# Kernel optimization log

Hardware: AMD Instinct MI355X
Metric: run time of the kernel (lower is better)

The kernel has to match this reference:

```python
import jax, jax.numpy as jnp
import numpy as np

B, T, D, H, E = 2, 1024, 1024, 4096, 8


def setup_inputs() -> dict:
    key = jax.random.key(0)
    ks = jax.random.split(key, 7)
    s = 0.02  # weight init scale
    return {
        "x": jax.random.normal(ks[0], (B, T, D), jnp.float32),
        "gate_w": jax.random.normal(ks[1], (D, E), jnp.float32) * s,
        "gate_b": jnp.zeros((E,), jnp.float32),
        "w1": jax.random.normal(ks[2], (E, D, H), jnp.float32) * s,
        "b1": jnp.zeros((E, H), jnp.float32),
        "w2": jax.random.normal(ks[3], (E, H, D), jnp.float32) * s,
        "b2": jnp.zeros((E, D), jnp.float32),
    }


def reference(x, gate_w, gate_b, w1, b1, w2, b2):
    b, t, d = x.shape
    e = gate_w.shape[1]
    xt = x.reshape(b * t, d)                      # [N, D]
    logits = xt @ gate_w + gate_b                 # [N, E]
    probs = jax.nn.softmax(logits, axis=-1)
    top_expert = jnp.argmax(probs, axis=-1)       # [N]
    onehot = jax.nn.one_hot(top_expert, e, dtype=x.dtype)  # [N, E]
    # dense per-expert FFN, then combine via top-1 one-hot (same math as masked dispatch)
    h = jax.nn.gelu(jnp.einsum('nd,edh->enh', xt, w1) + b1[:, None, :], approximate=False)  # [E, N, H]
    y = jnp.einsum('enh,ehd->end', h, w2) + b2[:, None, :]                                  # [E, N, D]
    out = jnp.einsum('end,ne->nd', y, onehot).reshape(b, t, d)
    counts = jnp.sum(onehot, axis=0)              # [E], float
    frac = counts / jnp.maximum(counts.sum(), 1.0)
    aux_loss = jnp.mean((frac - 1.0 / e) ** 2)
    return out, aux_loss
```

## Files before the change

kernel.cpp:

```cpp
#include <hip/hip_runtime.h>
#include <stdint.h>

#define N_TOK 2048
#define DDIM 1024
#define HDIM 4096
#define NEXP 8
#define BM 128
#define MAXT 24
#define PADCAP 3072

#define C_COUNTS 0
#define C_CURSOR 8
#define C_PADOFF 16
#define C_TILECNT 25
#define C_TILE_E 32
#define C_TILE_M0 56
#define C_TILE_ROWS 80
#define C_EXPERT 128
#define C_PERM 2176

#define XG_OFF 32768
#define HG_OFF (XG_OFF + PADCAP*DDIM*2)

typedef float f32x4 __attribute__((ext_vector_type(4)));
typedef short s16x8 __attribute__((ext_vector_type(8)));
typedef unsigned int u32;
typedef unsigned short u16;

__device__ __forceinline__ u16 f2bf(float f){
  u32 u = __float_as_uint(f);
  u += 0x7fffu + ((u >> 16) & 1u);
  return (u16)(u >> 16);
}

__device__ __forceinline__ u32 pkbf(float a, float b){
  u32 r; asm("v_cvt_pk_bf16_f32 %0, %1, %2" : "=v"(r) : "v"(a), "v"(b)); return r;
}

__device__ __forceinline__ void gl_lds16(const void* g, void* l){
  __builtin_amdgcn_global_load_lds((const __attribute__((address_space(1))) u32*)g,
                                   (__attribute__((address_space(3))) u32*)l, 16, 0, 0);
}

__global__ __launch_bounds__(256) void gate_kern(
    const float* __restrict__ x, const float* __restrict__ gw,
    const float* __restrict__ gb, int* __restrict__ ctrl)
{
  const int wv = threadIdx.x >> 6, l = threadIdx.x & 63;
  const int n = blockIdx.x * 4 + wv;
  const float* xr = x + (size_t)n * DDIM;
  float acc[NEXP];
  #pragma unroll
  for (int e = 0; e < NEXP; e++) acc[e] = 0.f;
  #pragma unroll 4
  for (int i = 0; i < DDIM/64; i++){
    int k = i*64 + l;
    float xv = xr[k];
    const float* g = gw + (size_t)k * NEXP;
    #pragma unroll
    for (int e = 0; e < NEXP; e++) acc[e] = fmaf(xv, g[e], acc[e]);
  }
  #pragma unroll
  for (int e = 0; e < NEXP; e++){
    #pragma unroll
    for (int off = 32; off > 0; off >>= 1) acc[e] += __shfl_xor(acc[e], off);
  }
  if (l == 0){
    float best = acc[0] + gb[0]; int bi = 0;
    #pragma unroll
    for (int e = 1; e < NEXP; e++){
      float v = acc[e] + gb[e];
      if (v > best){ best = v; bi = e; }
    }
    ctrl[C_EXPERT + n] = bi;
    atomicAdd(&ctrl[C_COUNTS + bi], 1);
  }
}

__global__ void setup_kern(int* __restrict__ ctrl, float* __restrict__ aux_out)
{
  const int t = threadIdx.x;
  for (int i = t; i < PADCAP; i += 256) ctrl[C_PERM + i] = -1;
  if (t == 0){
    int off = 0, tc = 0;
    float aux = 0.f;
    for (int e = 0; e < NEXP; e++){
      int c = ctrl[C_COUNTS + e];
      ctrl[C_PADOFF + e] = off;
      ctrl[C_CURSOR + e] = off;
      int nt = (c + BM - 1) / BM;
      for (int j = 0; j < nt; j++){
        ctrl[C_TILE_E   + tc] = e;
        ctrl[C_TILE_M0  + tc] = off + j*BM;
        ctrl[C_TILE_ROWS+ tc] = min(BM, c - j*BM);
        tc++;
      }
      off += nt * BM;
      float fr = (float)c * (1.f/(float)N_TOK);
      float d = fr - 1.f/(float)NEXP;
      aux += d*d;
    }
    ctrl[C_TILECNT] = tc;
    *aux_out = aux * (1.f/(float)NEXP);
  }
}

__global__ __launch_bounds__(256) void scatter_kern(int* __restrict__ ctrl)
{
  const int n = blockIdx.x * 256 + threadIdx.x;
  const int e = ctrl[C_EXPERT + n];
  const int pos = atomicAdd(&ctrl[C_CURSOR + e], 1);
  ctrl[C_PERM + pos] = n;
}

__global__ __launch_bounds__(256) void xg_kern(
    const float* __restrict__ x, const int* __restrict__ ctrl,
    u16* __restrict__ Xg)
{
  const int slot = blockIdx.x, t = threadIdx.x;
  const int tok = ctrl[C_PERM + slot];
  ushort4 o;
  if (tok >= 0){
    f32x4 v = *(const f32x4*)(x + (size_t)tok*DDIM + t*4);
    o.x = f2bf(v.x); o.y = f2bf(v.y); o.z = f2bf(v.z); o.w = f2bf(v.w);
  } else { o.x = 0; o.y = 0; o.z = 0; o.w = 0; }
  *(ushort4*)(Xg + (size_t)slot*DDIM + t*4) = o;
}

template<int MODE>
__global__ __launch_bounds__(256, 4) void moe_gemm(
    const u16* __restrict__ Ag, const float* __restrict__ W,
    const float* __restrict__ bias, u16* __restrict__ Hg,
    float* __restrict__ outp, const int* __restrict__ ctrl)
{
  constexpr int K    = (MODE==1) ? DDIM : HDIM;
  constexpr int NN   = (MODE==1) ? HDIM : DDIM;
  constexpr int KS   = (MODE==1) ? 1 : 4;
  constexpr int KLOC = K / KS;
  constexpr int BN   = 64;
  constexpr int BK   = 32;
  constexpr int NF   = BN / 32;
  constexpr int CPR  = BK / 8;
  constexpr int AVM  = (BM*BK)/(256*8);
  constexpr int BCPR = BN / 4;
  constexpr int BVM  = (BK*BN)/(256*4);
  constexpr int NT   = KLOC / BK;

  const int by = blockIdx.y;
  if (by >= ctrl[C_TILECNT]) return;
  const int e    = ctrl[C_TILE_E + by];
  const int m0   = ctrl[C_TILE_M0 + by];
  const int rows = ctrl[C_TILE_ROWS + by];
  const int n0   = blockIdx.x * BN;
  const int kb   = (MODE==1) ? 0 : blockIdx.z * KLOC;

  const int tid = threadIdx.x;
  const int w = tid >> 6, l = tid & 63;
  const int wr = w >> 1, wc = w & 1;
  const int lhi = l >> 4, llo = l & 15;

  __shared__ __align__(16) u16   As[2][BM*BK];
  __shared__ __align__(16) float Bs[2][BK*BN];
  __shared__ int perm_s[BM];

  if constexpr (MODE == 2){
    if (tid < BM) perm_s[tid] = ctrl[C_PERM + m0 + tid];
  }

  f32x4 acc[4][NF];
  #pragma unroll
  for (int mf = 0; mf < 4; mf++)
    #pragma unroll
    for (int nf = 0; nf < NF; nf++) acc[mf][nf] = (f32x4){0.f,0.f,0.f,0.f};

  const u16* Abase = Ag + (size_t)m0 * K;
  int arow[AVM], apos[AVM];
  #pragma unroll
  for (int i = 0; i < AVM; i++){
    int f = i*256 + tid;
    arow[i] = f / CPR;
    apos[i] = (f & (CPR-1)) ^ (arow[i] & (CPR-1));
  }
  const float* Wb = W + (size_t)e * K * NN + n0;
  int brow[BVM], bpos[BVM];
  #pragma unroll
  for (int i = 0; i < BVM; i++){
    int f = i*256 + tid;
    brow[i] = f / BCPR;
    bpos[i] = (f % BCPR) ^ (((brow[i] >> 3) & 1) << 2);
  }

  const int col0 = wc*(BN/2) + llo;
  const int bswz = (lhi & 1) << 2;

#define STAGE_A(buf, k0) { \
    u16* ad = &As[buf][(w*64)*8]; \
    _Pragma("unroll") \
    for (int i = 0; i < AVM; i++) \
      gl_lds16(Abase + (size_t)arow[i]*K + (k0) + apos[i]*8, ad + i*256*8); }

#define STAGE_B(buf, k0) { \
    float* bd = &Bs[buf][(w*64)*4]; \
    _Pragma("unroll") \
    for (int i = 0; i < BVM; i++) \
      gl_lds16(Wb + (size_t)((k0) + brow[i])*NN + bpos[i]*4, bd + i*256*4); }

#define COMPUTE(buf) { \
    s16x8 a[4]; \
    _Pragma("unroll") \
    for (int mf = 0; mf < 4; mf++){ \
      int row = wr*64 + mf*16 + llo; \
      int pos = lhi ^ (row & (CPR-1)); \
      a[mf] = *(const s16x8*)&As[buf][row*BK + pos*8]; } \
    _Pragma("unroll") \
    for (int nf = 0; nf < NF; nf++){ \
      const int col = col0 + nf*16; \
      const float* bp_ = &Bs[buf][(lhi*8)*BN + \
                                  ((((col) >> 2) ^ bswz) << 2) + ((col) & 3)]; \
      union { u32 u[4]; s16x8 v; } bb_; \
      bb_.u[0] = pkbf(bp_[0*BN], bp_[1*BN]); \
      bb_.u[1] = pkbf(bp_[2*BN], bp_[3*BN]); \
      bb_.u[2] = pkbf(bp_[4*BN], bp_[5*BN]); \
      bb_.u[3] = pkbf(bp_[6*BN], bp_[7*BN]); \
      _Pragma("unroll") \
      for (int mf = 0; mf < 4; mf++) \
        acc[mf][nf] = __builtin_amdgcn_mfma_f32_16x16x32_bf16(a[mf], bb_.v, acc[mf][nf], 0, 0, 0); \
    } }

  STAGE_A(0, kb);
  STAGE_B(0, kb);
  __syncthreads();

  int cur = 0;
  #pragma unroll 1
  for (int t = 0; t < NT; t++){
    if (t+1 < NT){
      STAGE_A(cur^1, kb + (t+1)*BK);
      STAGE_B(cur^1, kb + (t+1)*BK);
    }
    COMPUTE(cur);
    __syncthreads();
    cur ^= 1;
  }

  if constexpr (MODE == 1){
    const float* bp = bias + (size_t)e*NN + n0;
    #pragma unroll
    for (int nf = 0; nf < NF; nf++){
      const int cl = wc*(BN/2) + nf*16 + llo;
      const float bb = bp[cl];
      #pragma unroll
      for (int mf = 0; mf < 4; mf++){
        #pragma unroll
        for (int r = 0; r < 4; r++){
          const int rl = wr*64 + mf*16 + lhi*4 + r;
          float vv = acc[mf][nf][r] + bb;
          float gel = 0.5f * vv * (1.0f + erff(vv * 0.70710678118f));
          Hg[(size_t)(m0+rl)*NN + n0 + cl] = f2bf(gel);
        }
      }
    }
  } else {
    const float* bp = bias + (size_t)e*NN + n0;
    const bool addb = (blockIdx.z == 0);
    #pragma unroll
    for (int mf = 0; mf < 4; mf++){
      #pragma unroll
      for (int r = 0; r < 4; r++){
        const int rl = wr*64 + mf*16 + lhi*4 + r;
        if (rl < rows){
          const int tok = perm_s[rl];
          #pragma unroll
          for (int nf = 0; nf < NF; nf++){
            const int cl = wc*(BN/2) + nf*16 + llo;
            float v = acc[mf][nf][r] + (addb ? bp[cl] : 0.f);
            atomicAdd(&outp[(size_t)tok*DDIM + n0 + cl], v);
          }
        }
      }
    }
  }
#undef STAGE_A
#undef STAGE_B
#undef COMPUTE
}

extern "C" void kernel_launch(void* const* d_in, const int* in_sizes, int n_in,
                              void* d_out, int out_size, void* d_ws, size_t ws_size,
                              hipStream_t stream)
{
  (void)in_sizes; (void)n_in; (void)out_size; (void)ws_size;
  const float* x  = (const float*)d_in[0];
  const float* gw = (const float*)d_in[1];
  const float* gb = (const float*)d_in[2];
  const float* w1 = (const float*)d_in[3];
  const float* b1 = (const float*)d_in[4];
  const float* w2 = (const float*)d_in[5];
  const float* b2 = (const float*)d_in[6];
  float* out = (float*)d_out;
  char* ws = (char*)d_ws;
  int* ctrl = (int*)ws;
  u16* Xg = (u16*)(ws + XG_OFF);
  u16* Hg = (u16*)(ws + HG_OFF);

  hipMemsetAsync(ctrl, 0, 64, stream);
  hipMemsetAsync(out, 0, (size_t)N_TOK*DDIM*4, stream);
  gate_kern<<<N_TOK/4, 256, 0, stream>>>(x, gw, gb, ctrl);
  setup_kern<<<1, 256, 0, stream>>>(ctrl, out + (size_t)N_TOK*DDIM);
  scatter_kern<<<N_TOK/256, 256, 0, stream>>>(ctrl);
  xg_kern<<<PADCAP, 256, 0, stream>>>(x, ctrl, Xg);
  moe_gemm<1><<<dim3(HDIM/64, MAXT),    256, 0, stream>>>(Xg, w1, b1, Hg, nullptr, ctrl);
  moe_gemm<2><<<dim3(DDIM/64, MAXT, 4), 256, 0, stream>>>(Hg, w2, b2, nullptr, out, ctrl);
}
```

Measured before the change: 238.4 us.

## Load GEMM operands directly from global into registers, dropping LDS staging

```diff
diff --git a/kernel.cpp b/kernel.cpp
--- a/kernel.cpp
+++ b/kernel.cpp
@@ -35,11 +35,6 @@
 
 __device__ __forceinline__ u32 pkbf(float a, float b){
   u32 r; asm("v_cvt_pk_bf16_f32 %0, %1, %2" : "=v"(r) : "v"(a), "v"(b)); return r;
-}
-
-__device__ __forceinline__ void gl_lds16(const void* g, void* l){
-  __builtin_amdgcn_global_load_lds((const __attribute__((address_space(1))) u32*)g,
-                                   (__attribute__((address_space(3))) u32*)l, 16, 0, 0);
 }
 
 __global__ __launch_bounds__(256) void gate_kern(
@@ -128,7 +123,7 @@
 }
 
 template<int MODE>
-__global__ __launch_bounds__(256, 4) void moe_gemm(
+__global__ __launch_bounds__(256, 3) void moe_gemm(
     const u16* __restrict__ Ag, const float* __restrict__ W,
     const float* __restrict__ bias, u16* __restrict__ Hg,
     float* __restrict__ outp, const int* __restrict__ ctrl)
@@ -140,10 +135,6 @@
   constexpr int BN   = 64;
   constexpr int BK   = 32;
   constexpr int NF   = BN / 32;
-  constexpr int CPR  = BK / 8;
-  constexpr int AVM  = (BM*BK)/(256*8);
-  constexpr int BCPR = BN / 4;
-  constexpr int BVM  = (BK*BN)/(256*4);
   constexpr int NT   = KLOC / BK;
 
   const int by = blockIdx.y;
@@ -159,95 +150,59 @@
   const int wr = w >> 1, wc = w & 1;
   const int lhi = l >> 4, llo = l & 15;
 
-  __shared__ __align__(16) u16   As[2][BM*BK];
-  __shared__ __align__(16) float Bs[2][BK*BN];
-  __shared__ int perm_s[BM];
-
-  if constexpr (MODE == 2){
-    if (tid < BM) perm_s[tid] = ctrl[C_PERM + m0 + tid];
-  }
-
   f32x4 acc[4][NF];
   #pragma unroll
   for (int mf = 0; mf < 4; mf++)
     #pragma unroll
     for (int nf = 0; nf < NF; nf++) acc[mf][nf] = (f32x4){0.f,0.f,0.f,0.f};
 
-  const u16* Abase = Ag + (size_t)m0 * K;
-  int arow[AVM], apos[AVM];
-  #pragma unroll
-  for (int i = 0; i < AVM; i++){
-    int f = i*256 + tid;
-    arow[i] = f / CPR;
-    apos[i] = (f & (CPR-1)) ^ (arow[i] & (CPR-1));
-  }
-  const float* Wb = W + (size_t)e * K * NN + n0;
-  int brow[BVM], bpos[BVM];
-  #pragma unroll
-  for (int i = 0; i < BVM; i++){
-    int f = i*256 + tid;
-    brow[i] = f / BCPR;
-    bpos[i] = (f % BCPR) ^ (((brow[i] >> 3) & 1) << 2);
-  }
-
-  const int col0 = wc*(BN/2) + llo;
-  const int bswz = (lhi & 1) << 2;
-
-#define STAGE_A(buf, k0) { \
-    u16* ad = &As[buf][(w*64)*8]; \
+  const u16* Arow = Ag + (size_t)(m0 + wr*64 + llo) * K + lhi*8;
+  const float* Wc = W + (size_t)e * K * NN + n0 + wc*32 + llo;
+
+  s16x8 af0[4], af1[4];
+  float bw0[NF*8], bw1[NF*8];
+
+#define LOADA(AF, k0) { \
     _Pragma("unroll") \
-    for (int i = 0; i < AVM; i++) \
-      gl_lds16(Abase + (size_t)arow[i]*K + (k0) + apos[i]*8, ad + i*256*8); }
-
-#define STAGE_B(buf, k0) { \
-    float* bd = &Bs[buf][(w*64)*4]; \
-    _Pragma("unroll") \
-    for (int i = 0; i < BVM; i++) \
-      gl_lds16(Wb + (size_t)((k0) + brow[i])*NN + bpos[i]*4, bd + i*256*4); }
-
-#define COMPUTE(buf) { \
-    s16x8 a[4]; \
-    _Pragma("unroll") \
-    for (int mf = 0; mf < 4; mf++){ \
-      int row = wr*64 + mf*16 + llo; \
-      int pos = lhi ^ (row & (CPR-1)); \
-      a[mf] = *(const s16x8*)&As[buf][row*BK + pos*8]; } \
+    for (int mf = 0; mf < 4; mf++) \
+      AF[mf] = *(const s16x8*)(Arow + (size_t)mf*16*K + (k0)); }
+
+#define LOADB(BW, k0) { \
     _Pragma("unroll") \
     for (int nf = 0; nf < NF; nf++){ \
-      const int col = col0 + nf*16; \
-      const float* bp_ = &Bs[buf][(lhi*8)*BN + \
-                                  ((((col) >> 2) ^ bswz) << 2) + ((col) & 3)]; \
+      const float* wp = Wc + (size_t)((k0) + lhi*8) * NN + nf*16; \
+      _Pragma("unroll") \
+      for (int j = 0; j < 8; j++) \
+        BW[nf*8+j] = wp[(size_t)j * NN]; } }
+
+#define COMP(AF, BW) { \
+    _Pragma("unroll") \
+    for (int nf = 0; nf < NF; nf++){ \
       union { u32 u[4]; s16x8 v; } bb_; \
-      bb_.u[0] = pkbf(bp_[0*BN], bp_[1*BN]); \
-      bb_.u[1] = pkbf(bp_[2*BN], bp_[3*BN]); \
-      bb_.u[2] = pkbf(bp_[4*BN], bp_[5*BN]); \
-      bb_.u[3] = pkbf(bp_[6*BN], bp_[7*BN]); \
+      bb_.u[0] = pkbf(BW[nf*8+0], BW[nf*8+1]); \
+      bb_.u[1] = pkbf(BW[nf*8+2], BW[nf*8+3]); \
+      bb_.u[2] = pkbf(BW[nf*8+4], BW[nf*8+5]); \
+      bb_.u[3] = pkbf(BW[nf*8+6], BW[nf*8+7]); \
       _Pragma("unroll") \
       for (int mf = 0; mf < 4; mf++) \
-        acc[mf][nf] = __builtin_amdgcn_mfma_f32_16x16x32_bf16(a[mf], bb_.v, acc[mf][nf], 0, 0, 0); \
-    } }
-
-  STAGE_A(0, kb);
-  STAGE_B(0, kb);
-  __syncthreads();
-
-  int cur = 0;
+        acc[mf][nf] = __builtin_amdgcn_mfma_f32_16x16x32_bf16(AF[mf], bb_.v, acc[mf][nf], 0, 0, 0); } }
+
+  LOADA(af0, kb);
+  LOADB(bw0, kb);
+
   #pragma unroll 1
-  for (int t = 0; t < NT; t++){
-    if (t+1 < NT){
-      STAGE_A(cur^1, kb + (t+1)*BK);
-      STAGE_B(cur^1, kb + (t+1)*BK);
-    }
-    COMPUTE(cur);
-    __syncthreads();
-    cur ^= 1;
+  for (int t = 0; t < NT; t += 2){
+    if (t+1 < NT){ LOADA(af1, kb + (t+1)*BK); LOADB(bw1, kb + (t+1)*BK); }
+    COMP(af0, bw0);
+    if (t+2 < NT){ LOADA(af0, kb + (t+2)*BK); LOADB(bw0, kb + (t+2)*BK); }
+    if (t+1 < NT){ COMP(af1, bw1); }
   }
 
   if constexpr (MODE == 1){
     const float* bp = bias + (size_t)e*NN + n0;
     #pragma unroll
     for (int nf = 0; nf < NF; nf++){
-      const int cl = wc*(BN/2) + nf*16 + llo;
+      const int cl = wc*32 + nf*16 + llo;
       const float bb = bp[cl];
       #pragma unroll
       for (int mf = 0; mf < 4; mf++){
@@ -269,10 +224,10 @@
       for (int r = 0; r < 4; r++){
         const int rl = wr*64 + mf*16 + lhi*4 + r;
         if (rl < rows){
-          const int tok = perm_s[rl];
+          const int tok = ctrl[C_PERM + m0 + rl];
           #pragma unroll
           for (int nf = 0; nf < NF; nf++){
-            const int cl = wc*(BN/2) + nf*16 + llo;
+            const int cl = wc*32 + nf*16 + llo;
             float v = acc[mf][nf][r] + (addb ? bp[cl] : 0.f);
             atomicAdd(&outp[(size_t)tok*DDIM + n0 + cl], v);
           }
@@ -280,9 +235,9 @@
       }
     }
   }
-#undef STAGE_A
-#undef STAGE_B
-#undef COMPUTE
+#undef LOADA
+#undef LOADB
+#undef COMP
 }
 
 extern "C" void kernel_launch(void* const* d_in, const int* in_sizes, int n_in,
```

New measurement: 339.8 us. 1.43x slower.

## Triple-buffer GEMM LDS staging with partial vmcnt waits and MFMA priority

Applied to the files above, without the earlier changes.

```diff
diff --git a/kernel.cpp b/kernel.cpp
--- a/kernel.cpp
+++ b/kernel.cpp
@@ -128,7 +128,7 @@
 }
 
 template<int MODE>
-__global__ __launch_bounds__(256, 4) void moe_gemm(
+__global__ __launch_bounds__(256, 3) void moe_gemm(
     const u16* __restrict__ Ag, const float* __restrict__ W,
     const float* __restrict__ bias, u16* __restrict__ Hg,
     float* __restrict__ outp, const int* __restrict__ ctrl)
@@ -159,8 +159,8 @@
   const int wr = w >> 1, wc = w & 1;
   const int lhi = l >> 4, llo = l & 15;
 
-  __shared__ __align__(16) u16   As[2][BM*BK];
-  __shared__ __align__(16) float Bs[2][BK*BN];
+  __shared__ __align__(16) u16   As[3][BM*BK];
+  __shared__ __align__(16) float Bs[3][BK*BN];
   __shared__ int perm_s[BM];
 
   if constexpr (MODE == 2){
@@ -179,7 +179,7 @@
   for (int i = 0; i < AVM; i++){
     int f = i*256 + tid;
     arow[i] = f / CPR;
-    apos[i] = (f & (CPR-1)) ^ (arow[i] & (CPR-1));
+    apos[i] = (f & (CPR-1)) ^ (arow[i] & (CPR-1)) ^ (((arow[i] >> 2) & 1) << 1);
   }
   const float* Wb = W + (size_t)e * K * NN + n0;
   int brow[BVM], bpos[BVM];
@@ -192,6 +192,12 @@
 
   const int col0 = wc*(BN/2) + llo;
   const int bswz = (lhi & 1) << 2;
+
+#define WAITV(N) asm volatile("s_waitcnt vmcnt(" #N ")" ::: "memory")
+#define PIPE_BAR() do { asm volatile("s_waitcnt lgkmcnt(0)" ::: "memory"); \
+    __builtin_amdgcn_sched_barrier(0); \
+    __builtin_amdgcn_s_barrier(); \
+    __builtin_amdgcn_sched_barrier(0); } while(0)
 
 #define STAGE_A(buf, k0) { \
     u16* ad = &As[buf][(w*64)*8]; \
@@ -210,8 +216,9 @@
     _Pragma("unroll") \
     for (int mf = 0; mf < 4; mf++){ \
       int row = wr*64 + mf*16 + llo; \
-      int pos = lhi ^ (row & (CPR-1)); \
+      int pos = (lhi ^ (row & (CPR-1))) ^ (((row >> 2) & 1) << 1); \
       a[mf] = *(const s16x8*)&As[buf][row*BK + pos*8]; } \
+    __builtin_amdgcn_s_setprio(1); \
     _Pragma("unroll") \
     for (int nf = 0; nf < NF; nf++){ \
       const int col = col0 + nf*16; \
@@ -225,22 +232,28 @@
       _Pragma("unroll") \
       for (int mf = 0; mf < 4; mf++) \
         acc[mf][nf] = __builtin_amdgcn_mfma_f32_16x16x32_bf16(a[mf], bb_.v, acc[mf][nf], 0, 0, 0); \
-    } }
+    } \
+    __builtin_amdgcn_s_setprio(0); }
 
   STAGE_A(0, kb);
   STAGE_B(0, kb);
-  __syncthreads();
-
-  int cur = 0;
+  STAGE_A(1, kb + BK);
+  STAGE_B(1, kb + BK);
+  WAITV(4);
+  PIPE_BAR();
+
+  int cbuf = 0, sbuf = 2;
   #pragma unroll 1
   for (int t = 0; t < NT; t++){
-    if (t+1 < NT){
-      STAGE_A(cur^1, kb + (t+1)*BK);
-      STAGE_B(cur^1, kb + (t+1)*BK);
-    }
-    COMPUTE(cur);
-    __syncthreads();
-    cur ^= 1;
+    if (t+2 < NT){
+      STAGE_A(sbuf, kb + (t+2)*BK);
+      STAGE_B(sbuf, kb + (t+2)*BK);
+    }
+    COMPUTE(cbuf);
+    if (t+2 < NT){ WAITV(4); } else { WAITV(0); }
+    PIPE_BAR();
+    cbuf = (cbuf==2) ? 0 : cbuf+1;
+    sbuf = (sbuf==2) ? 0 : sbuf+1;
   }
 
   if constexpr (MODE == 1){
@@ -280,6 +293,8 @@
       }
     }
   }
+#undef WAITV
+#undef PIPE_BAR
 #undef STAGE_A
 #undef STAGE_B
 #undef COMPUTE
```

Measured after the change: 232.8 us. -2.4%, faster.

## Enlarge MoE GEMM tiles, pack weights to bf16 in LDS, compact token layout

Applied to the files above, without the earlier changes.

```diff
diff --git a/kernel.cpp b/kernel.cpp
--- a/kernel.cpp
+++ b/kernel.cpp
@@ -5,9 +5,9 @@
 #define DDIM 1024
 #define HDIM 4096
 #define NEXP 8
-#define BM 128
-#define MAXT 24
-#define PADCAP 3072
+#define BM 256
+#define MAXT 16
+#define ACAP 2560
 
 #define C_COUNTS 0
 #define C_CURSOR 8
@@ -20,11 +20,12 @@
 #define C_PERM 2176
 
 #define XG_OFF 32768
-#define HG_OFF (XG_OFF + PADCAP*DDIM*2)
+#define HG_OFF (XG_OFF + ACAP*DDIM*2)
 
 typedef float f32x4 __attribute__((ext_vector_type(4)));
 typedef short s16x8 __attribute__((ext_vector_type(8)));
 typedef unsigned int u32;
+typedef u32 u32x2 __attribute__((ext_vector_type(2)));
 typedef unsigned short u16;
 
 __device__ __forceinline__ u16 f2bf(float f){
@@ -80,7 +81,7 @@
 __global__ void setup_kern(int* __restrict__ ctrl, float* __restrict__ aux_out)
 {
   const int t = threadIdx.x;
-  for (int i = t; i < PADCAP; i += 256) ctrl[C_PERM + i] = -1;
+  for (int i = t; i < 3072; i += 256) ctrl[C_PERM + i] = -1;
   if (t == 0){
     int off = 0, tc = 0;
     float aux = 0.f;
@@ -95,7 +96,7 @@
         ctrl[C_TILE_ROWS+ tc] = min(BM, c - j*BM);
         tc++;
       }
-      off += nt * BM;
+      off += c;
       float fr = (float)c * (1.f/(float)N_TOK);
       float d = fr - 1.f/(float)NEXP;
       aux += d*d;
@@ -128,7 +129,7 @@
 }
 
 template<int MODE>
-__global__ __launch_bounds__(256, 4) void moe_gemm(
+__global__ __launch_bounds__(512, 2) void moe_gemm(
     const u16* __restrict__ Ag, const float* __restrict__ W,
     const float* __restrict__ bias, u16* __restrict__ Hg,
     float* __restrict__ outp, const int* __restrict__ ctrl)
@@ -137,13 +138,8 @@
   constexpr int NN   = (MODE==1) ? HDIM : DDIM;
   constexpr int KS   = (MODE==1) ? 1 : 4;
   constexpr int KLOC = K / KS;
-  constexpr int BN   = 64;
+  constexpr int BN   = 128;
   constexpr int BK   = 32;
-  constexpr int NF   = BN / 32;
-  constexpr int CPR  = BK / 8;
-  constexpr int AVM  = (BM*BK)/(256*8);
-  constexpr int BCPR = BN / 4;
-  constexpr int BVM  = (BK*BN)/(256*4);
   constexpr int NT   = KLOC / BK;
 
   const int by = blockIdx.y;
@@ -159,86 +155,86 @@
   const int wr = w >> 1, wc = w & 1;
   const int lhi = l >> 4, llo = l & 15;
 
-  __shared__ __align__(16) u16   As[2][BM*BK];
-  __shared__ __align__(16) float Bs[2][BK*BN];
+  __shared__ __align__(16) u16 As[2][BM*BK];
+  __shared__ __align__(16) u16 Bs[2][BN*BK];
   __shared__ int perm_s[BM];
 
   if constexpr (MODE == 2){
     if (tid < BM) perm_s[tid] = ctrl[C_PERM + m0 + tid];
   }
 
-  f32x4 acc[4][NF];
+  f32x4 acc[4][4];
   #pragma unroll
   for (int mf = 0; mf < 4; mf++)
     #pragma unroll
-    for (int nf = 0; nf < NF; nf++) acc[mf][nf] = (f32x4){0.f,0.f,0.f,0.f};
+    for (int nf = 0; nf < 4; nf++) acc[mf][nf] = (f32x4){0.f,0.f,0.f,0.f};
 
   const u16* Abase = Ag + (size_t)m0 * K;
-  int arow[AVM], apos[AVM];
+  int arow[2], apos[2];
   #pragma unroll
-  for (int i = 0; i < AVM; i++){
-    int f = i*256 + tid;
-    arow[i] = f / CPR;
-    apos[i] = (f & (CPR-1)) ^ (arow[i] & (CPR-1));
-  }
-  const float* Wb = W + (size_t)e * K * NN + n0;
-  int brow[BVM], bpos[BVM];
-  #pragma unroll
-  for (int i = 0; i < BVM; i++){
-    int f = i*256 + tid;
-    brow[i] = f / BCPR;
-    bpos[i] = (f % BCPR) ^ (((brow[i] >> 3) & 1) << 2);
-  }
-
-  const int col0 = wc*(BN/2) + llo;
-  const int bswz = (lhi & 1) << 2;
+  for (int i = 0; i < 2; i++){
+    int f = i*512 + tid;
+    arow[i] = f >> 2;
+    apos[i] = (f & 3) ^ (arow[i] & 3) ^ (((arow[i] >> 2) & 1) << 1);
+  }
+  const int bn  = tid & 127;
+  const int bkg = tid >> 7;
+  const int bsw = (bn >> 1) & 7;
+  const float* Wn = W + (size_t)e * K * NN + n0 + bn;
+  float wreg[8];
 
 #define STAGE_A(buf, k0) { \
     u16* ad = &As[buf][(w*64)*8]; \
     _Pragma("unroll") \
-    for (int i = 0; i < AVM; i++) \
-      gl_lds16(Abase + (size_t)arow[i]*K + (k0) + apos[i]*8, ad + i*256*8); }
-
-#define STAGE_B(buf, k0) { \
-    float* bd = &Bs[buf][(w*64)*4]; \
+    for (int i = 0; i < 2; i++) \
+      gl_lds16(Abase + (size_t)arow[i]*K + (k0) + apos[i]*8, ad + i*512*8); }
+
+#define BLOAD(k0) { \
     _Pragma("unroll") \
-    for (int i = 0; i < BVM; i++) \
-      gl_lds16(Wb + (size_t)((k0) + brow[i])*NN + bpos[i]*4, bd + i*256*4); }
+    for (int i = 0; i < 8; i++) \
+      wreg[i] = Wn[(size_t)((k0) + bkg*8 + i) * NN]; }
+
+#define BPACK(buf) { \
+    u32 p0 = pkbf(wreg[0], wreg[1]), p1 = pkbf(wreg[2], wreg[3]); \
+    u32 p2 = pkbf(wreg[4], wreg[5]), p3 = pkbf(wreg[6], wreg[7]); \
+    u16* bd = &Bs[buf][bn*BK]; \
+    *(u32x2*)&bd[((2*bkg)   ^ bsw) << 2] = (u32x2){p0, p1}; \
+    *(u32x2*)&bd[((2*bkg+1) ^ bsw) << 2] = (u32x2){p2, p3}; }
 
 #define COMPUTE(buf) { \
     s16x8 a[4]; \
     _Pragma("unroll") \
     for (int mf = 0; mf < 4; mf++){ \
       int row = wr*64 + mf*16 + llo; \
-      int pos = lhi ^ (row & (CPR-1)); \
+      int pos = (lhi ^ (row & 3)) ^ (((row >> 2) & 1) << 1); \
       a[mf] = *(const s16x8*)&As[buf][row*BK + pos*8]; } \
     _Pragma("unroll") \
-    for (int nf = 0; nf < NF; nf++){ \
-      const int col = col0 + nf*16; \
-      const float* bp_ = &Bs[buf][(lhi*8)*BN + \
-                                  ((((col) >> 2) ^ bswz) << 2) + ((col) & 3)]; \
-      union { u32 u[4]; s16x8 v; } bb_; \
-      bb_.u[0] = pkbf(bp_[0*BN], bp_[1*BN]); \
-      bb_.u[1] = pkbf(bp_[2*BN], bp_[3*BN]); \
-      bb_.u[2] = pkbf(bp_[4*BN], bp_[5*BN]); \
-      bb_.u[3] = pkbf(bp_[6*BN], bp_[7*BN]); \
+    for (int nf = 0; nf < 4; nf++){ \
+      const int col = wc*64 + nf*16 + llo; \
+      const int sw = (col >> 1) & 7; \
+      const u16* bb = &Bs[buf][col*BK]; \
+      union { u32 u[4]; s16x8 v; } bfr; \
+      *(u32x2*)&bfr.u[0] = *(const u32x2*)&bb[((2*lhi)   ^ sw) << 2]; \
+      *(u32x2*)&bfr.u[2] = *(const u32x2*)&bb[((2*lhi+1) ^ sw) << 2]; \
       _Pragma("unroll") \
       for (int mf = 0; mf < 4; mf++) \
-        acc[mf][nf] = __builtin_amdgcn_mfma_f32_16x16x32_bf16(a[mf], bb_.v, acc[mf][nf], 0, 0, 0); \
+        acc[mf][nf] = __builtin_amdgcn_mfma_f32_16x16x32_bf16(a[mf], bfr.v, acc[mf][nf], 0, 0, 0); \
     } }
 
+  BLOAD(kb);
   STAGE_A(0, kb);
-  STAGE_B(0, kb);
+  BPACK(0);
   __syncthreads();
 
   int cur = 0;
   #pragma unroll 1
   for (int t = 0; t < NT; t++){
     if (t+1 < NT){
+      BLOAD(kb + (t+1)*BK);
       STAGE_A(cur^1, kb + (t+1)*BK);
-      STAGE_B(cur^1, kb + (t+1)*BK);
     }
     COMPUTE(cur);
+    if (t+1 < NT){ BPACK(cur^1); }
     __syncthreads();
     cur ^= 1;
   }
@@ -246,17 +242,19 @@
   if constexpr (MODE == 1){
     const float* bp = bias + (size_t)e*NN + n0;
     #pragma unroll
-    for (int nf = 0; nf < NF; nf++){
-      const int cl = wc*(BN/2) + nf*16 + llo;
+    for (int nf = 0; nf < 4; nf++){
+      const int cl = wc*64 + nf*16 + llo;
       const float bb = bp[cl];
       #pragma unroll
       for (int mf = 0; mf < 4; mf++){
         #pragma unroll
         for (int r = 0; r < 4; r++){
           const int rl = wr*64 + mf*16 + lhi*4 + r;
-          float vv = acc[mf][nf][r] + bb;
-          float gel = 0.5f * vv * (1.0f + erff(vv * 0.70710678118f));
-          Hg[(size_t)(m0+rl)*NN + n0 + cl] = f2bf(gel);
+          if (rl < rows){
+            float vv = acc[mf][nf][r] + bb;
+            float gel = 0.5f * vv * (1.0f + erff(vv * 0.70710678118f));
+            Hg[(size_t)(m0+rl)*NN + n0 + cl] = f2bf(gel);
+          }
         }
       }
     }
@@ -271,8 +269,8 @@
         if (rl < rows){
           const int tok = perm_s[rl];
           #pragma unroll
-          for (int nf = 0; nf < NF; nf++){
-            const int cl = wc*(BN/2) + nf*16 + llo;
+          for (int nf = 0; nf < 4; nf++){
+            const int cl = wc*64 + nf*16 + llo;
             float v = acc[mf][nf][r] + (addb ? bp[cl] : 0.f);
             atomicAdd(&outp[(size_t)tok*DDIM + n0 + cl], v);
           }
@@ -281,7 +279,8 @@
     }
   }
 #undef STAGE_A
-#undef STAGE_B
+#undef BLOAD
+#undef BPACK
 #undef COMPUTE
 }
 
@@ -308,7 +307,7 @@
   gate_kern<<<N_TOK/4, 256, 0, stream>>>(x, gw, gb, ctrl);
   setup_kern<<<1, 256, 0, stream>>>(ctrl, out + (size_t)N_TOK*DDIM);
   scatter_kern<<<N_TOK/256, 256, 0, stream>>>(ctrl);
-  xg_kern<<<PADCAP, 256, 0, stream>>>(x, ctrl, Xg);
-  moe_gemm<1><<<dim3(HDIM/64, MAXT),    256, 0, stream>>>(Xg, w1, b1, Hg, nullptr, ctrl);
-  moe_gemm<2><<<dim3(DDIM/64, MAXT, 4), 256, 0, stream>>>(Hg, w2, b2, nullptr, out, ctrl);
-}
+  xg_kern<<<N_TOK, 256, 0, stream>>>(x, ctrl, Xg);
+  moe_gemm<1><<<dim3(HDIM/128, MAXT),    512, 0, stream>>>(Xg, w1, b1, Hg, nullptr, ctrl);
+  moe_gemm<2><<<dim3(DDIM/128, MAXT, 4), 512, 0, stream>>>(Hg, w2, b2, nullptr, out, ctrl);
+}
```

Measured after the change: 216.4 us. -9.2%, faster.
